# Optimization experiments

Measured on AMD Instinct MI355X. Metric: run time of the kernel, lower is better.

Reference implementation:

```python
import jax, jax.numpy as jnp
import numpy as np

D = 192          # d_model
H = 8            # n_heads
DH = D // H      # d_head = 24
DFF = 2 * D      # FeedForward hidden = d_model*2
SIZES = [384 + 8 * i for i in range(32)]   # ragged segment lengths
TOTAL = sum(SIZES)                          # 16256
EPS = 1e-5

# static ragged -> padded index maps (numpy, baked at trace time)
_sz = np.asarray(SIZES)
B = len(_sz)
MAXN = int(_sz.max())
SEG = np.repeat(np.arange(B), _sz)                      # [TOTAL] segment id
POS = np.concatenate([np.arange(s) for s in _sz])       # [TOTAL] position in segment
PADMASK = np.ones((B, MAXN), dtype=bool)                # True = padding (key_padding_mask)
PADMASK[SEG, POS] = False


def _layernorm(x, gamma, beta):
    mu = jnp.mean(x, axis=-1, keepdims=True)
    var = jnp.var(x, axis=-1, keepdims=True)
    return (x - mu) * jax.lax.rsqrt(var + EPS) * gamma + beta


def setup_inputs() -> dict:
    key = jax.random.key(0)
    ks = jax.random.split(key, 8)
    w = lambda k, shape: jax.random.normal(k, shape, jnp.float32) * 0.02
    return {
        "x": jax.random.normal(ks[0], (TOTAL, D), jnp.float32),
        "sizes": jnp.asarray(SIZES, jnp.int32),
        "Wqkv": w(ks[1], (3 * D, D)), "bqkv": jnp.zeros((3 * D,), jnp.float32),
        "Wo": w(ks[2], (D, D)),       "bo": jnp.zeros((D,), jnp.float32),
        "Wg": w(ks[3], (D, 2 * D)),   "bg": jnp.zeros((D,), jnp.float32),
        "gamma1": jnp.ones((D,), jnp.float32), "beta1": jnp.zeros((D,), jnp.float32),
        "W1": w(ks[4], (DFF, D)),     "b1": jnp.zeros((DFF,), jnp.float32),
        "W2": w(ks[5], (D, DFF)),     "b2": jnp.zeros((D,), jnp.float32),
        "gamma2": jnp.ones((D,), jnp.float32), "beta2": jnp.zeros((D,), jnp.float32),
    }


def reference(x, sizes, Wqkv, bqkv, Wo, bo, Wg, bg, gamma1, beta1,
              W1, b1, W2, b2, gamma2, beta2):
    # --- pad_by_sizes (vectorized scatter, static index maps) ---
    pad = jnp.zeros((B, MAXN, D), x.dtype).at[SEG, POS].set(x)   # [B, MAXN, D]

    # --- nn.MultiheadAttention (batch_first, key_padding_mask) ---
    qkv = pad @ Wqkv.T + bqkv                                    # [B, MAXN, 3D]
    q, k, v = jnp.split(qkv, 3, axis=-1)
    def heads(t):  # [B, MAXN, D] -> [B, H, MAXN, DH]
        return t.reshape(B, MAXN, H, DH).transpose(0, 2, 1, 3)
    q, k, v = heads(q), heads(k), heads(v)
    scores = jnp.einsum("bhqd,bhkd->bhqk", q, k) / np.sqrt(DH)   # [B, H, MAXN, MAXN]
    scores = jnp.where(PADMASK[:, None, None, :], jnp.float32(-1e9), scores)
    attn = jax.nn.softmax(scores, axis=-1)
    o = jnp.einsum("bhqk,bhkd->bhqd", attn, v)                   # [B, H, MAXN, DH]
    o = o.transpose(0, 2, 1, 3).reshape(B, MAXN, D)
    out = o @ Wo.T + bo                                          # [B, MAXN, D]

    # --- gather back to ragged; gate/norm/ff are per-token, so the torch
    # per-segment loop is equivalent to one vectorized pass over all tokens ---
    out_flat = out[SEG, POS]                                     # [TOTAL, D]
    g = jax.nn.sigmoid(jnp.concatenate([out_flat, x], axis=-1) @ Wg.T + bg)
    h = g * out_flat + (1.0 - g) * x                             # GatedResidual
    h = _layernorm(h, gamma1, beta1)                             # self.norm
    y = jax.nn.silu(h @ W1.T + b1) @ W2.T + b2                   # FeedForward.net
    return _layernorm(h + y, gamma2, beta2)                      # residual + norm
```

## Files before the change

### kernel.cpp

```cpp
#include <hip/hip_runtime.h>
#include <math.h>

#define D_      192
#define H_      8
#define DH_     24
#define NSEG    32
#define TOTAL_  16256
static constexpr float LN_EPS = 1e-5f;
static constexpr float SCALE  = 0.20412414523193154f;
static constexpr float SC_L2E = 0.29446679331797463f;

typedef float  f32x4  __attribute__((ext_vector_type(4)));
typedef short  bf16x8 __attribute__((ext_vector_type(8)));
typedef unsigned short u16x4 __attribute__((ext_vector_type(4)));
typedef unsigned int   u32x4 __attribute__((ext_vector_type(4)));

__device__ __forceinline__ unsigned short f2b(float f) {
    union { float f; unsigned u; } v; v.f = f;
    unsigned r = v.u + 0x7FFFu + ((v.u >> 16) & 1u);
    return (unsigned short)(r >> 16);
}
__device__ __forceinline__ unsigned f2b_u32(float f) {
    union { float f; unsigned u; } v; v.f = f;
    return (v.u + 0x8000u) >> 16;
}
__device__ __forceinline__ unsigned short f2b_fast(float f) {
    union { float f; unsigned u; } v; v.f = f;
    return (unsigned short)((v.u + 0x8000u) >> 16);
}
__device__ __forceinline__ float b2f(unsigned short h) {
    union { unsigned u; float f; } v; v.u = (unsigned)h << 16; return v.f;
}
__device__ __forceinline__ float fexp2(float x) {
#if __has_builtin(__builtin_amdgcn_exp2f)
    return __builtin_amdgcn_exp2f(x);
#else
    return exp2f(x);
#endif
}
__device__ __forceinline__ bf16x8 ldpack8(const float* p) {
    float4 a0 = *(const float4*)p;
    float4 a1 = *(const float4*)(p + 4);
    bf16x8 r;
    ((unsigned short*)&r)[0] = f2b(a0.x); ((unsigned short*)&r)[1] = f2b(a0.y);
    ((unsigned short*)&r)[2] = f2b(a0.z); ((unsigned short*)&r)[3] = f2b(a0.w);
    ((unsigned short*)&r)[4] = f2b(a1.x); ((unsigned short*)&r)[5] = f2b(a1.y);
    ((unsigned short*)&r)[6] = f2b(a1.z); ((unsigned short*)&r)[7] = f2b(a1.w);
    return r;
}

#define NXE 3121152
__global__ __launch_bounds__(256)
void conv_all(const float* __restrict__ x,
              const float* __restrict__ w0, const float* __restrict__ w1,
              const float* __restrict__ w2, const float* __restrict__ w3,
              const float* __restrict__ w4,
              unsigned short* __restrict__ xb, unsigned short* __restrict__ wb)
{
    int i = (blockIdx.x * 256 + threadIdx.x) * 4;
    const float* src; unsigned short* dst; int off;
    if (i < NXE) { src = x; dst = xb; off = 0; }
    else {
        int j = i - NXE; dst = wb;
        if      (j < 110592) { src = w0; off = 0; }
        else if (j < 147456) { src = w1; off = 110592; }
        else if (j < 221184) { src = w2; off = 147456; }
        else if (j < 294912) { src = w3; off = 221184; }
        else                 { src = w4; off = 294912; }
        i = j;
    }
    float4 v = *(const float4*)&src[i - off];
    u16x4 o = { f2b(v.x), f2b(v.y), f2b(v.z), f2b(v.w) };
    *(u16x4*)&dst[i] = o;
}

template<int KF, int MR, int OUT_BF16>
__global__ __launch_bounds__(256)
void gemm_lds(const unsigned short* __restrict__ Ain,
              const unsigned short* __restrict__ Wb,
              const float* __restrict__ bias,
              void* __restrict__ Cout, int N)
{
    constexpr int KSW = KF * 32 + 8;
    __shared__ unsigned short Wp[64 * KSW];

    const int tid = threadIdx.x;
    const int wv  = tid >> 6;
    const int l   = tid & 63;
    const int m0  = blockIdx.x * (64 * MR) + wv * (16 * MR);
    const int n0  = blockIdx.y * 64;
    const int rl  = l & 15;
    const int kc  = (l >> 4) * 8;

    bf16x8 afrag[MR][KF];
    #pragma unroll
    for (int h = 0; h < MR; ++h)
        #pragma unroll
        for (int kk = 0; kk < KF; ++kk)
            afrag[h][kk] = *(const bf16x8*)&Ain[(size_t)(m0 + h * 16 + rl) * (KF * 32) + kk * 32 + kc];

    #pragma unroll
    for (int i = 0; i < KF; ++i) {
        int u = i * 256 + tid;
        int row = u / (KF * 4), c = u % (KF * 4);
        *(bf16x8*)&Wp[row * KSW + c * 8] = *(const bf16x8*)&Wb[(size_t)(n0 + row) * (KF * 32) + c * 8];
    }
    __syncthreads();

    f32x4 acc[MR][4] = {};
    #pragma unroll
    for (int kk = 0; kk < KF; ++kk) {
        #pragma unroll
        for (int nf = 0; nf < 4; ++nf) {
            bf16x8 b = *(const bf16x8*)&Wp[(nf * 16 + rl) * KSW + kk * 32 + kc];
            #pragma unroll
            for (int h = 0; h < MR; ++h)
                acc[h][nf] = __builtin_amdgcn_mfma_f32_16x16x32_bf16(afrag[h][kk], b, acc[h][nf], 0, 0, 0);
        }
    }

    #pragma unroll
    for (int h = 0; h < MR; ++h) {
        #pragma unroll
        for (int nf = 0; nf < 4; ++nf) {
            const int c = n0 + nf * 16 + rl;
            const float bz = bias[c];
            #pragma unroll
            for (int q = 0; q < 4; ++q) {
                const int r = m0 + h * 16 + (l >> 4) * 4 + q;
                float v = acc[h][nf][q] + bz;
                if (OUT_BF16) ((unsigned short*)Cout)[(size_t)r * N + c] = f2b(v);
                else          ((float*)Cout)[(size_t)r * N + c] = v;
            }
        }
    }
}

__global__ __launch_bounds__(256, 1)
void wo_gate_ln1(const unsigned short* __restrict__ o_b,
                 const float* __restrict__ x,
                 const unsigned short* __restrict__ wo_b,
                 const unsigned short* __restrict__ wg_b,
                 const float* __restrict__ bo, const float* __restrict__ bg,
                 const float* __restrict__ gamma1, const float* __restrict__ beta1,
                 float* __restrict__ h1, unsigned short* __restrict__ h1b)
{
    constexpr int WS = 200;
    constexpr int AS = 200;
    __shared__ unsigned short Wp[192 * WS];
    __shared__ unsigned short Al[64 * AS];

    const int tid = threadIdx.x;
    const int wv  = tid >> 6;
    const int l   = tid & 63;
    const int rl  = l & 15;
    const int g   = l >> 4;
    const int kc  = g * 8;
    const int m0  = blockIdx.x * 64 + wv * 16;

    bf16x8 afA[6];
    #pragma unroll
    for (int kk = 0; kk < 6; ++kk)
        afA[kk] = *(const bf16x8*)&o_b[(size_t)(m0 + rl) * 192 + kk * 32 + kc];

    #pragma unroll
    for (int i = 0; i < 18; ++i) {
        int u = i * 256 + tid;
        int row = u / 24, c = u % 24;
        *(bf16x8*)&Wp[row * WS + c * 8] = *(const bf16x8*)&wo_b[(size_t)row * 192 + c * 8];
    }
    __syncthreads();

    f32x4 accA[12] = {};
    #pragma unroll
    for (int kk = 0; kk < 6; ++kk)
        #pragma unroll
        for (int nf = 0; nf < 12; ++nf) {
            bf16x8 b = *(const bf16x8*)&Wp[(nf * 16 + rl) * WS + kk * 32 + kc];
            accA[nf] = __builtin_amdgcn_mfma_f32_16x16x32_bf16(afA[kk], b, accA[nf], 0, 0, 0);
        }

    float att[12][4];
    #pragma unroll
    for (int nf = 0; nf < 12; ++nf) {
        const float bz = bo[nf * 16 + rl];
        #pragma unroll
        for (int q = 0; q < 4; ++q) {
            att[nf][q] = accA[nf][q] + bz;
            const int row = wv * 16 + g * 4 + q;
            Al[row * AS + nf * 16 + rl] = f2b(att[nf][q]);
        }
    }
    __syncthreads();

    #pragma unroll
    for (int i = 0; i < 18; ++i) {
        int u = i * 256 + tid;
        int row = u / 24, c = u % 24;
        *(bf16x8*)&Wp[row * WS + c * 8] = *(const bf16x8*)&wg_b[(size_t)row * 384 + c * 8];
    }
    __syncthreads();

    f32x4 accB[12] = {};
    #pragma unroll
    for (int kk = 0; kk < 6; ++kk) {
        bf16x8 a = *(const bf16x8*)&Al[(wv * 16 + rl) * AS + kk * 32 + kc];
        #pragma unroll
        for (int nf = 0; nf < 12; ++nf) {
            bf16x8 b = *(const bf16x8*)&Wp[(nf * 16 + rl) * WS + kk * 32 + kc];
            accB[nf] = __builtin_amdgcn_mfma_f32_16x16x32_bf16(a, b, accB[nf], 0, 0, 0);
        }
    }
    __syncthreads();

    #pragma unroll
    for (int i = 0; i < 18; ++i) {
        int u = i * 256 + tid;
        int row = u / 24, c = u % 24;
        *(bf16x8*)&Wp[row * WS + c * 8] = *(const bf16x8*)&wg_b[(size_t)row * 384 + 192 + c * 8];
    }
    __syncthreads();

    #pragma unroll
    for (int kk = 0; kk < 6; ++kk) {
        bf16x8 a = ldpack8(&x[(size_t)(m0 + rl) * 192 + kk * 32 + kc]);
        #pragma unroll
        for (int nf = 0; nf < 12; ++nf) {
            bf16x8 b = *(const bf16x8*)&Wp[(nf * 16 + rl) * WS + kk * 32 + kc];
            accB[nf] = __builtin_amdgcn_mfma_f32_16x16x32_bf16(a, b, accB[nf], 0, 0, 0);
        }
    }

    float bz[12], gam[12], bet[12];
    #pragma unroll
    for (int nf = 0; nf < 12; ++nf) {
        bz[nf]  = bg[nf * 16 + rl];
        gam[nf] = gamma1[nf * 16 + rl];
        bet[nf] = beta1[nf * 16 + rl];
    }
    #pragma unroll
    for (int q = 0; q < 4; ++q) {
        const int r = m0 + g * 4 + q;
        const size_t rb = (size_t)r * 192;
        float h[12];
        float s = 0.f;
        #pragma unroll
        for (int nf = 0; nf < 12; ++nf) {
            const int c = nf * 16 + rl;
            float v  = accB[nf][q] + bz[nf];
            float gt = 1.f / (1.f + __expf(-v));
            h[nf] = gt * att[nf][q] + (1.f - gt) * x[rb + c];
            s += h[nf];
        }
        s += __shfl_xor(s, 1); s += __shfl_xor(s, 2);
        s += __shfl_xor(s, 4); s += __shfl_xor(s, 8);
        const float mu = s * (1.f / 192.f);
        float sq = 0.f;
        #pragma unroll
        for (int nf = 0; nf < 12; ++nf) { float d = h[nf] - mu; sq += d * d; }
        sq += __shfl_xor(sq, 1); sq += __shfl_xor(sq, 2);
        sq += __shfl_xor(sq, 4); sq += __shfl_xor(sq, 8);
        const float rstd = rsqrtf(sq * (1.f / 192.f) + LN_EPS);
        #pragma unroll
        for (int nf = 0; nf < 12; ++nf) {
            const int c = nf * 16 + rl;
            float rv = (h[nf] - mu) * rstd * gam[nf] + bet[nf];
            h1[rb + c]  = rv;
            h1b[rb + c] = f2b(rv);
        }
    }
}

__global__ __launch_bounds__(256, 1)
void ffn_ln2(const unsigned short* __restrict__ h1b,
             const float* __restrict__ h1,
             const unsigned short* __restrict__ w1_b,
             const unsigned short* __restrict__ w2_b,
             const float* __restrict__ b1, const float* __restrict__ b2,
             const float* __restrict__ gamma2, const float* __restrict__ beta2,
             float* __restrict__ out)
{
    constexpr int WS = 200;
    constexpr int FS = 392;
    __shared__ unsigned short Wp[192 * WS];
    __shared__ unsigned short Fl[64 * FS];

    const int tid = threadIdx.x;
    const int wv  = tid >> 6;
    const int l   = tid & 63;
    const int rl  = l & 15;
    const int g   = l >> 4;
    const int kc  = g * 8;
    const int m0  = blockIdx.x * 64 + wv * 16;

    bf16x8 afC[6];
    #pragma unroll
    for (int kk = 0; kk < 6; ++kk)
        afC[kk] = *(const bf16x8*)&h1b[(size_t)(m0 + rl) * 192 + kk * 32 + kc];

    f32x4 accC[24] = {};
    #pragma unroll
    for (int ch = 0; ch < 2; ++ch) {
        if (ch) __syncthreads();
        #pragma unroll
        for (int i = 0; i < 18; ++i) {
            int u = i * 256 + tid;
            int row = u / 24, c = u % 24;
            *(bf16x8*)&Wp[row * WS + c * 8] = *(const bf16x8*)&w1_b[(size_t)(ch * 192 + row) * 192 + c * 8];
        }
        __syncthreads();
        #pragma unroll
        for (int kk = 0; kk < 6; ++kk)
            #pragma unroll
            for (int nf = 0; nf < 12; ++nf) {
                bf16x8 b = *(const bf16x8*)&Wp[(nf * 16 + rl) * WS + kk * 32 + kc];
                accC[ch * 12 + nf] = __builtin_amdgcn_mfma_f32_16x16x32_bf16(afC[kk], b, accC[ch * 12 + nf], 0, 0, 0);
            }
    }
    #pragma unroll
    for (int ch = 0; ch < 2; ++ch)
        #pragma unroll
        for (int nf = 0; nf < 12; ++nf) {
            const int col = ch * 192 + nf * 16 + rl;
            const float bz = b1[col];
            #pragma unroll
            for (int q = 0; q < 4; ++q) {
                float v = accC[ch * 12 + nf][q] + bz;
                float s = 1.f / (1.f + __expf(-v));
                const int row = wv * 16 + g * 4 + q;
                Fl[row * FS + col] = f2b(v * s);
            }
        }
    __syncthreads();

    f32x4 accD[12] = {};
    #pragma unroll
    for (int ch = 0; ch < 2; ++ch) {
        if (ch) __syncthreads();
        #pragma unroll
        for (int i = 0; i < 18; ++i) {
            int u = i * 256 + tid;
            int row = u / 24, c = u % 24;
            *(bf16x8*)&Wp[row * WS + c * 8] = *(const bf16x8*)&w2_b[(size_t)row * 384 + ch * 192 + c * 8];
        }
        __syncthreads();
        #pragma unroll
        for (int kk = 0; kk < 6; ++kk) {
            bf16x8 a = *(const bf16x8*)&Fl[(wv * 16 + rl) * FS + ch * 192 + kk * 32 + kc];
            #pragma unroll
            for (int nf = 0; nf < 12; ++nf) {
                bf16x8 b = *(const bf16x8*)&Wp[(nf * 16 + rl) * WS + kk * 32 + kc];
                accD[nf] = __builtin_amdgcn_mfma_f32_16x16x32_bf16(a, b, accD[nf], 0, 0, 0);
            }
        }
    }

    float bz[12], gam[12], bet[12];
    #pragma unroll
    for (int nf = 0; nf < 12; ++nf) {
        bz[nf]  = b2[nf * 16 + rl];
        gam[nf] = gamma2[nf * 16 + rl];
        bet[nf] = beta2[nf * 16 + rl];
    }
    #pragma unroll
    for (int q = 0; q < 4; ++q) {
        const int r = m0 + g * 4 + q;
        const size_t rb = (size_t)r * 192;
        float h[12];
        float s = 0.f;
        #pragma unroll
        for (int nf = 0; nf < 12; ++nf) {
            const int c = nf * 16 + rl;
            h[nf] = h1[rb + c] + accD[nf][q] + bz[nf];
            s += h[nf];
        }
        s += __shfl_xor(s, 1); s += __shfl_xor(s, 2);
        s += __shfl_xor(s, 4); s += __shfl_xor(s, 8);
        const float mu = s * (1.f / 192.f);
        float sq = 0.f;
        #pragma unroll
        for (int nf = 0; nf < 12; ++nf) { float d = h[nf] - mu; sq += d * d; }
        sq += __shfl_xor(sq, 1); sq += __shfl_xor(sq, 2);
        sq += __shfl_xor(sq, 4); sq += __shfl_xor(sq, 8);
        const float rstd = rsqrtf(sq * (1.f / 192.f) + LN_EPS);
        #pragma unroll
        for (int nf = 0; nf < 12; ++nf) {
            const int c = nf * 16 + rl;
            out[rb + c] = (h[nf] - mu) * rstd * gam[nf] + bet[nf];
        }
    }
}

#define KSTR 40
#define VSTR 72

__global__ __launch_bounds__(256)
void attn_mfma(const unsigned short* __restrict__ qkv, unsigned short* __restrict__ o)
{
    const int seg  = blockIdx.z;
    const int head = blockIdx.y;
    const int n    = 384 + 8 * seg;
    const int base = 384 * seg + 4 * seg * (seg - 1);
    const int q0   = blockIdx.x * 128;
    if (q0 >= n) return;

    __shared__ unsigned short Ks[64 * KSTR];
    __shared__ unsigned short Vt[32 * VSTR];

    const int tid = threadIdx.x;
    const int wv  = tid >> 6;
    const int l   = tid & 63;
    const int lq  = l & 15;
    const int g   = l >> 4;

    if (tid < 64) *(uint4*)&Ks[tid * KSTR + 24] = make_uint4(0, 0, 0, 0);
    for (int t4 = tid; t4 < 144; t4 += 256)
        *(unsigned long long*)&Vt[24 * VSTR + t4 * 4] = 0ull;

    int   qrow[2];
    bf16x8 qfrag[2];
    #pragma unroll
    for (int qf = 0; qf < 2; ++qf) {
        qrow[qf] = q0 + wv * 32 + qf * 16 + lq;
        const int qtok = base + (qrow[qf] < n ? qrow[qf] : n - 1);
        bf16x8 qz = {};
        if (g < 3) qz = *(const bf16x8*)&qkv[(size_t)qtok * 576 + head * 24 + g * 8];
        qfrag[qf] = qz;
    }

    float lsum[2] = {0.f, 0.f};
    f32x4 oacc[2][2] = {};

    const int nt = (n + 63) >> 6;
    for (int t = 0; t < nt; ++t) {
        const int j0 = t * 64;
        __syncthreads();
        if (tid < 192) {
            const int j = tid & 63;
            const int c = tid >> 6;
            const int cj = 32 * (j >> 5) + 8 * ((j >> 2) & 3) + 4 * ((j >> 4) & 1) + (j & 3);
            int jr = j0 + j; if (jr >= n) jr = n - 1;
            const unsigned short* rp = &qkv[(size_t)(base + jr) * 576 + head * 24 + c * 8];
            bf16x8 kv = *(const bf16x8*)(rp + 192);
            *(bf16x8*)&Ks[j * KSTR + c * 8] = kv;
            bf16x8 vv = *(const bf16x8*)(rp + 384);
            #pragma unroll
            for (int e = 0; e < 8; ++e)
                Vt[(c * 8 + e) * VSTR + cj] = ((const unsigned short*)&vv)[e];
        }
        __syncthreads();

        bf16x8 kf[4];
        #pragma unroll
        for (int ks = 0; ks < 4; ++ks)
            kf[ks] = *(const bf16x8*)&Ks[(ks * 16 + lq) * KSTR + g * 8];

        const int rem = n - j0;
        bf16x8 pfr[2][2];
        #pragma unroll
        for (int qf = 0; qf < 2; ++qf) {
            f32x4 sacc[4] = {};
            #pragma unroll
            for (int ks = 0; ks < 4; ++ks)
                sacc[ks] = __builtin_amdgcn_mfma_f32_16x16x32_bf16(kf[ks], qfrag[qf], sacc[ks], 0, 0, 0);

            float psum = 0.f;
            unsigned pw[8];
            #pragma unroll
            for (int ks = 0; ks < 4; ++ks) {
                float pv[4];
                #pragma unroll
                for (int r = 0; r < 4; ++r) {
                    float p = fexp2(sacc[ks][r] * SC_L2E);
                    if (rem < 64) { int key = ks * 16 + g * 4 + r; if (key >= rem) p = 0.f; }
                    psum += p;
                    pv[r] = p;
                }
                pw[ks * 2 + 0] = f2b_u32(pv[0]) | (f2b_u32(pv[1]) << 16);
                pw[ks * 2 + 1] = f2b_u32(pv[2]) | (f2b_u32(pv[3]) << 16);
            }
            psum += __shfl_xor(psum, 16);
            psum += __shfl_xor(psum, 32);
            lsum[qf] += psum;
            #pragma unroll
            for (int jk = 0; jk < 2; ++jk) {
                u32x4 fr = { pw[jk*4+0], pw[jk*4+1], pw[jk*4+2], pw[jk*4+3] };
                pfr[qf][jk] = *(bf16x8*)&fr;
            }
        }

        #pragma unroll
        for (int jk = 0; jk < 2; ++jk) {
            bf16x8 vf[2];
            #pragma unroll
            for (int df = 0; df < 2; ++df)
                vf[df] = *(const bf16x8*)&Vt[(df * 16 + lq) * VSTR + jk * 32 + g * 8];
            #pragma unroll
            for (int qf = 0; qf < 2; ++qf)
                #pragma unroll
                for (int df = 0; df < 2; ++df)
                    oacc[qf][df] = __builtin_amdgcn_mfma_f32_16x16x32_bf16(vf[df], pfr[qf][jk], oacc[qf][df], 0, 0, 0);
        }
    }

    #pragma unroll
    for (int qf = 0; qf < 2; ++qf) {
        if (qrow[qf] < n) {
            const float rl2 = 1.f / lsum[qf];
            #pragma unroll
            for (int df = 0; df < 2; ++df) {
                const int d0 = df * 16 + g * 4;
                if (d0 < 24) {
                    u16x4 r = { f2b_fast(oacc[qf][df][0] * rl2), f2b_fast(oacc[qf][df][1] * rl2),
                                f2b_fast(oacc[qf][df][2] * rl2), f2b_fast(oacc[qf][df][3] * rl2) };
                    *(u16x4*)&o[(size_t)(base + qrow[qf]) * 192 + head * 24 + d0] = r;
                }
            }
        }
    }
}

extern "C" void kernel_launch(void* const* d_in, const int* in_sizes, int n_in,
                              void* d_out, int out_size, void* d_ws, size_t ws_size,
                              hipStream_t stream)
{
    const float* x      = (const float*)d_in[0];
    const float* Wqkv   = (const float*)d_in[2];
    const float* bqkv   = (const float*)d_in[3];
    const float* Wo     = (const float*)d_in[4];
    const float* bo     = (const float*)d_in[5];
    const float* Wg     = (const float*)d_in[6];
    const float* bg     = (const float*)d_in[7];
    const float* gamma1 = (const float*)d_in[8];
    const float* beta1  = (const float*)d_in[9];
    const float* W1     = (const float*)d_in[10];
    const float* b1     = (const float*)d_in[11];
    const float* W2     = (const float*)d_in[12];
    const float* b2     = (const float*)d_in[13];
    const float* gamma2 = (const float*)d_in[14];
    const float* beta2  = (const float*)d_in[15];
    float* out = (float*)d_out;
    float* ws  = (float*)d_ws;

    const size_t T = TOTAL_;
    unsigned short* qkv_b = (unsigned short*)ws;
    unsigned short* o_b   = (unsigned short*)(ws + 288 * T);
    float*          h1    = ws + 384 * T;
    unsigned short* h1b   = (unsigned short*)(ws + 576 * T);
    unsigned short* wb    = (unsigned short*)(ws + 672 * T);
    unsigned short* xb    = (unsigned short*)(ws + 684 * T);

    dim3 blk(256);

    conv_all<<<dim3(3408), blk, 0, stream>>>(x, Wqkv, Wo, Wg, W1, W2, xb, wb);
    gemm_lds<6,2,1><<<dim3(127, 9), blk, 0, stream>>>(xb, wb, bqkv, qkv_b, 576);
    attn_mfma<<<dim3(5, H_, NSEG), blk, 0, stream>>>(qkv_b, o_b);
    wo_gate_ln1<<<dim3(254), blk, 0, stream>>>(o_b, x, wb + 110592, wb + 147456,
                                               bo, bg, gamma1, beta1, h1, h1b);
    ffn_ln2<<<dim3(254), blk, 0, stream>>>(h1b, h1, wb + 221184, wb + 294912,
                                           b1, b2, gamma2, beta2, out);
}
```

Measured before the change: 97.69 us.

## Double-buffer attention K/V tiles, halve LDS in MLP kernels, drop fp32 intermediates

```diff
diff --git a/kernel.cpp b/kernel.cpp
--- a/kernel.cpp
+++ b/kernel.cpp
@@ -37,16 +37,6 @@
 #else
     return exp2f(x);
 #endif
-}
-__device__ __forceinline__ bf16x8 ldpack8(const float* p) {
-    float4 a0 = *(const float4*)p;
-    float4 a1 = *(const float4*)(p + 4);
-    bf16x8 r;
-    ((unsigned short*)&r)[0] = f2b(a0.x); ((unsigned short*)&r)[1] = f2b(a0.y);
-    ((unsigned short*)&r)[2] = f2b(a0.z); ((unsigned short*)&r)[3] = f2b(a0.w);
-    ((unsigned short*)&r)[4] = f2b(a1.x); ((unsigned short*)&r)[5] = f2b(a1.y);
-    ((unsigned short*)&r)[6] = f2b(a1.z); ((unsigned short*)&r)[7] = f2b(a1.w);
-    return r;
 }
 
 #define NXE 3121152
@@ -136,19 +126,18 @@
     }
 }
 
-__global__ __launch_bounds__(256, 1)
+__global__ __launch_bounds__(256, 2)
 void wo_gate_ln1(const unsigned short* __restrict__ o_b,
-                 const float* __restrict__ x,
+                 const unsigned short* __restrict__ xb,
                  const unsigned short* __restrict__ wo_b,
                  const unsigned short* __restrict__ wg_b,
                  const float* __restrict__ bo, const float* __restrict__ bg,
                  const float* __restrict__ gamma1, const float* __restrict__ beta1,
-                 float* __restrict__ h1, unsigned short* __restrict__ h1b)
+                 unsigned short* __restrict__ h1b)
 {
     constexpr int WS = 200;
-    constexpr int AS = 200;
-    __shared__ unsigned short Wp[192 * WS];
-    __shared__ unsigned short Al[64 * AS];
+    __shared__ unsigned short Wp[96 * WS];
+    __shared__ unsigned short Al[64 * WS];
 
     const int tid = threadIdx.x;
     const int wv  = tid >> 6;
@@ -163,80 +152,75 @@
     for (int kk = 0; kk < 6; ++kk)
         afA[kk] = *(const bf16x8*)&o_b[(size_t)(m0 + rl) * 192 + kk * 32 + kc];
 
-    #pragma unroll
-    for (int i = 0; i < 18; ++i) {
-        int u = i * 256 + tid;
-        int row = u / 24, c = u % 24;
-        *(bf16x8*)&Wp[row * WS + c * 8] = *(const bf16x8*)&wo_b[(size_t)row * 192 + c * 8];
-    }
-    __syncthreads();
-
     f32x4 accA[12] = {};
     #pragma unroll
-    for (int kk = 0; kk < 6; ++kk)
-        #pragma unroll
-        for (int nf = 0; nf < 12; ++nf) {
-            bf16x8 b = *(const bf16x8*)&Wp[(nf * 16 + rl) * WS + kk * 32 + kc];
-            accA[nf] = __builtin_amdgcn_mfma_f32_16x16x32_bf16(afA[kk], b, accA[nf], 0, 0, 0);
-        }
+    for (int sub = 0; sub < 2; ++sub) {
+        __syncthreads();
+        #pragma unroll
+        for (int i = 0; i < 9; ++i) {
+            int u = i * 256 + tid;
+            int row = u / 24, c = u % 24;
+            *(bf16x8*)&Wp[row * WS + c * 8] = *(const bf16x8*)&wo_b[(size_t)(sub * 96 + row) * 192 + c * 8];
+        }
+        __syncthreads();
+        #pragma unroll
+        for (int kk = 0; kk < 6; ++kk)
+            #pragma unroll
+            for (int nf2 = 0; nf2 < 6; ++nf2) {
+                bf16x8 b = *(const bf16x8*)&Wp[(nf2 * 16 + rl) * WS + kk * 32 + kc];
+                accA[sub * 6 + nf2] = __builtin_amdgcn_mfma_f32_16x16x32_bf16(afA[kk], b, accA[sub * 6 + nf2], 0, 0, 0);
+            }
+    }
 
     float att[12][4];
     #pragma unroll
     for (int nf = 0; nf < 12; ++nf) {
-        const float bz = bo[nf * 16 + rl];
+        const int cnf = (nf / 6) * 96 + (nf % 6) * 16 + rl;
+        const float bz = bo[cnf];
         #pragma unroll
         for (int q = 0; q < 4; ++q) {
             att[nf][q] = accA[nf][q] + bz;
-            const int row = wv * 16 + g * 4 + q;
-            Al[row * AS + nf * 16 + rl] = f2b(att[nf][q]);
-        }
-    }
-    __syncthreads();
-
-    #pragma unroll
-    for (int i = 0; i < 18; ++i) {
-        int u = i * 256 + tid;
-        int row = u / 24, c = u % 24;
-        *(bf16x8*)&Wp[row * WS + c * 8] = *(const bf16x8*)&wg_b[(size_t)row * 384 + c * 8];
-    }
-    __syncthreads();
+            Al[(wv * 16 + g * 4 + q) * WS + cnf] = f2b(att[nf][q]);
+        }
+    }
+
+    bf16x8 afX[6];
+    #pragma unroll
+    for (int kk = 0; kk < 6; ++kk)
+        afX[kk] = *(const bf16x8*)&xb[(size_t)(m0 + rl) * 192 + kk * 32 + kc];
 
     f32x4 accB[12] = {};
     #pragma unroll
-    for (int kk = 0; kk < 6; ++kk) {
-        bf16x8 a = *(const bf16x8*)&Al[(wv * 16 + rl) * AS + kk * 32 + kc];
-        #pragma unroll
-        for (int nf = 0; nf < 12; ++nf) {
-            bf16x8 b = *(const bf16x8*)&Wp[(nf * 16 + rl) * WS + kk * 32 + kc];
-            accB[nf] = __builtin_amdgcn_mfma_f32_16x16x32_bf16(a, b, accB[nf], 0, 0, 0);
-        }
-    }
-    __syncthreads();
-
-    #pragma unroll
-    for (int i = 0; i < 18; ++i) {
-        int u = i * 256 + tid;
-        int row = u / 24, c = u % 24;
-        *(bf16x8*)&Wp[row * WS + c * 8] = *(const bf16x8*)&wg_b[(size_t)row * 384 + 192 + c * 8];
-    }
-    __syncthreads();
-
-    #pragma unroll
-    for (int kk = 0; kk < 6; ++kk) {
-        bf16x8 a = ldpack8(&x[(size_t)(m0 + rl) * 192 + kk * 32 + kc]);
-        #pragma unroll
-        for (int nf = 0; nf < 12; ++nf) {
-            bf16x8 b = *(const bf16x8*)&Wp[(nf * 16 + rl) * WS + kk * 32 + kc];
-            accB[nf] = __builtin_amdgcn_mfma_f32_16x16x32_bf16(a, b, accB[nf], 0, 0, 0);
-        }
-    }
+    for (int kb = 0; kb < 2; ++kb)
+        #pragma unroll
+        for (int sub = 0; sub < 2; ++sub) {
+            __syncthreads();
+            #pragma unroll
+            for (int i = 0; i < 9; ++i) {
+                int u = i * 256 + tid;
+                int row = u / 24, c = u % 24;
+                *(bf16x8*)&Wp[row * WS + c * 8] = *(const bf16x8*)&wg_b[(size_t)(sub * 96 + row) * 384 + kb * 192 + c * 8];
+            }
+            __syncthreads();
+            #pragma unroll
+            for (int kk = 0; kk < 6; ++kk) {
+                bf16x8 a = (kb == 0) ? *(const bf16x8*)&Al[(wv * 16 + rl) * WS + kk * 32 + kc]
+                                     : afX[kk];
+                #pragma unroll
+                for (int nf2 = 0; nf2 < 6; ++nf2) {
+                    bf16x8 b = *(const bf16x8*)&Wp[(nf2 * 16 + rl) * WS + kk * 32 + kc];
+                    accB[sub * 6 + nf2] = __builtin_amdgcn_mfma_f32_16x16x32_bf16(a, b, accB[sub * 6 + nf2], 0, 0, 0);
+                }
+            }
+        }
 
     float bz[12], gam[12], bet[12];
     #pragma unroll
     for (int nf = 0; nf < 12; ++nf) {
-        bz[nf]  = bg[nf * 16 + rl];
-        gam[nf] = gamma1[nf * 16 + rl];
-        bet[nf] = beta1[nf * 16 + rl];
+        const int cnf = (nf / 6) * 96 + (nf % 6) * 16 + rl;
+        bz[nf]  = bg[cnf];
+        gam[nf] = gamma1[cnf];
+        bet[nf] = beta1[cnf];
     }
     #pragma unroll
     for (int q = 0; q < 4; ++q) {
@@ -246,10 +230,10 @@
         float s = 0.f;
         #pragma unroll
         for (int nf = 0; nf < 12; ++nf) {
-            const int c = nf * 16 + rl;
+            const int cnf = (nf / 6) * 96 + (nf % 6) * 16 + rl;
             float v  = accB[nf][q] + bz[nf];
             float gt = 1.f / (1.f + __expf(-v));
-            h[nf] = gt * att[nf][q] + (1.f - gt) * x[rb + c];
+            h[nf] = gt * att[nf][q] + (1.f - gt) * b2f(xb[rb + cnf]);
             s += h[nf];
         }
         s += __shfl_xor(s, 1); s += __shfl_xor(s, 2);
@@ -263,17 +247,14 @@
         const float rstd = rsqrtf(sq * (1.f / 192.f) + LN_EPS);
         #pragma unroll
         for (int nf = 0; nf < 12; ++nf) {
-            const int c = nf * 16 + rl;
-            float rv = (h[nf] - mu) * rstd * gam[nf] + bet[nf];
-            h1[rb + c]  = rv;
-            h1b[rb + c] = f2b(rv);
-        }
-    }
-}
-
-__global__ __launch_bounds__(256, 1)
+            const int cnf = (nf / 6) * 96 + (nf % 6) * 16 + rl;
+            h1b[rb + cnf] = f2b((h[nf] - mu) * rstd * gam[nf] + bet[nf]);
+        }
+    }
+}
+
+__global__ __launch_bounds__(256, 2)
 void ffn_ln2(const unsigned short* __restrict__ h1b,
-             const float* __restrict__ h1,
              const unsigned short* __restrict__ w1_b,
              const unsigned short* __restrict__ w2_b,
              const float* __restrict__ b1, const float* __restrict__ b2,
@@ -281,9 +262,8 @@
              float* __restrict__ out)
 {
     constexpr int WS = 200;
-    constexpr int FS = 392;
-    __shared__ unsigned short Wp[192 * WS];
-    __shared__ unsigned short Fl[64 * FS];
+    __shared__ unsigned short Wp[96 * WS];
+    __shared__ unsigned short Fl[64 * WS];
 
     const int tid = threadIdx.x;
     const int wv  = tid >> 6;
@@ -298,59 +278,57 @@
     for (int kk = 0; kk < 6; ++kk)
         afC[kk] = *(const bf16x8*)&h1b[(size_t)(m0 + rl) * 192 + kk * 32 + kc];
 
-    f32x4 accC[24] = {};
+    f32x4 accD[12] = {};
     #pragma unroll
     for (int ch = 0; ch < 2; ++ch) {
-        if (ch) __syncthreads();
-        #pragma unroll
-        for (int i = 0; i < 18; ++i) {
-            int u = i * 256 + tid;
-            int row = u / 24, c = u % 24;
-            *(bf16x8*)&Wp[row * WS + c * 8] = *(const bf16x8*)&w1_b[(size_t)(ch * 192 + row) * 192 + c * 8];
-        }
-        __syncthreads();
-        #pragma unroll
-        for (int kk = 0; kk < 6; ++kk)
-            #pragma unroll
-            for (int nf = 0; nf < 12; ++nf) {
-                bf16x8 b = *(const bf16x8*)&Wp[(nf * 16 + rl) * WS + kk * 32 + kc];
-                accC[ch * 12 + nf] = __builtin_amdgcn_mfma_f32_16x16x32_bf16(afC[kk], b, accC[ch * 12 + nf], 0, 0, 0);
-            }
-    }
-    #pragma unroll
-    for (int ch = 0; ch < 2; ++ch)
+        f32x4 accC[12] = {};
+        #pragma unroll
+        for (int sub = 0; sub < 2; ++sub) {
+            __syncthreads();
+            #pragma unroll
+            for (int i = 0; i < 9; ++i) {
+                int u = i * 256 + tid;
+                int row = u / 24, c = u % 24;
+                *(bf16x8*)&Wp[row * WS + c * 8] = *(const bf16x8*)&w1_b[(size_t)(ch * 192 + sub * 96 + row) * 192 + c * 8];
+            }
+            __syncthreads();
+            #pragma unroll
+            for (int kk = 0; kk < 6; ++kk)
+                #pragma unroll
+                for (int nf2 = 0; nf2 < 6; ++nf2) {
+                    bf16x8 b = *(const bf16x8*)&Wp[(nf2 * 16 + rl) * WS + kk * 32 + kc];
+                    accC[sub * 6 + nf2] = __builtin_amdgcn_mfma_f32_16x16x32_bf16(afC[kk], b, accC[sub * 6 + nf2], 0, 0, 0);
+                }
+        }
         #pragma unroll
         for (int nf = 0; nf < 12; ++nf) {
-            const int col = ch * 192 + nf * 16 + rl;
-            const float bz = b1[col];
+            const int colc = (nf / 6) * 96 + (nf % 6) * 16 + rl;
+            const float bz1 = b1[ch * 192 + colc];
             #pragma unroll
             for (int q = 0; q < 4; ++q) {
-                float v = accC[ch * 12 + nf][q] + bz;
+                float v = accC[nf][q] + bz1;
                 float s = 1.f / (1.f + __expf(-v));
-                const int row = wv * 16 + g * 4 + q;
-                Fl[row * FS + col] = f2b(v * s);
-            }
-        }
-    __syncthreads();
-
-    f32x4 accD[12] = {};
-    #pragma unroll
-    for (int ch = 0; ch < 2; ++ch) {
-        if (ch) __syncthreads();
-        #pragma unroll
-        for (int i = 0; i < 18; ++i) {
-            int u = i * 256 + tid;
-            int row = u / 24, c = u % 24;
-            *(bf16x8*)&Wp[row * WS + c * 8] = *(const bf16x8*)&w2_b[(size_t)row * 384 + ch * 192 + c * 8];
-        }
-        __syncthreads();
-        #pragma unroll
-        for (int kk = 0; kk < 6; ++kk) {
-            bf16x8 a = *(const bf16x8*)&Fl[(wv * 16 + rl) * FS + ch * 192 + kk * 32 + kc];
-            #pragma unroll
-            for (int nf = 0; nf < 12; ++nf) {
-                bf16x8 b = *(const bf16x8*)&Wp[(nf * 16 + rl) * WS + kk * 32 + kc];
-                accD[nf] = __builtin_amdgcn_mfma_f32_16x16x32_bf16(a, b, accD[nf], 0, 0, 0);
+                Fl[(wv * 16 + g * 4 + q) * WS + colc] = f2b(v * s);
+            }
+        }
+        #pragma unroll
+        for (int sub = 0; sub < 2; ++sub) {
+            __syncthreads();
+            #pragma unroll
+            for (int i = 0; i < 9; ++i) {
+                int u = i * 256 + tid;
+                int row = u / 24, c = u % 24;
+                *(bf16x8*)&Wp[row * WS + c * 8] = *(const bf16x8*)&w2_b[(size_t)(sub * 96 + row) * 384 + ch * 192 + c * 8];
+            }
+            __syncthreads();
+            #pragma unroll
+            for (int kk = 0; kk < 6; ++kk) {
+                bf16x8 a = *(const bf16x8*)&Fl[(wv * 16 + rl) * WS + kk * 32 + kc];
+                #pragma unroll
+                for (int nf2 = 0; nf2 < 6; ++nf2) {
+                    bf16x8 b = *(const bf16x8*)&Wp[(nf2 * 16 + rl) * WS + kk * 32 + kc];
+                    accD[sub * 6 + nf2] = __builtin_amdgcn_mfma_f32_16x16x32_bf16(a, b, accD[sub * 6 + nf2], 0, 0, 0);
+                }
             }
         }
     }
@@ -358,9 +336,10 @@
     float bz[12], gam[12], bet[12];
     #pragma unroll
     for (int nf = 0; nf < 12; ++nf) {
-        bz[nf]  = b2[nf * 16 + rl];
-        gam[nf] = gamma2[nf * 16 + rl];
-        bet[nf] = beta2[nf * 16 + rl];
+        const int cnf = (nf / 6) * 96 + (nf % 6) * 16 + rl;
+        bz[nf]  = b2[cnf];
+        gam[nf] = gamma2[cnf];
+        bet[nf] = beta2[cnf];
     }
     #pragma unroll
     for (int q = 0; q < 4; ++q) {
@@ -370,8 +349,8 @@
         float s = 0.f;
         #pragma unroll
         for (int nf = 0; nf < 12; ++nf) {
-            const int c = nf * 16 + rl;
-            h[nf] = h1[rb + c] + accD[nf][q] + bz[nf];
+            const int cnf = (nf / 6) * 96 + (nf % 6) * 16 + rl;
+            h[nf] = b2f(h1b[rb + cnf]) + accD[nf][q] + bz[nf];
             s += h[nf];
         }
         s += __shfl_xor(s, 1); s += __shfl_xor(s, 2);
@@ -385,8 +364,8 @@
         const float rstd = rsqrtf(sq * (1.f / 192.f) + LN_EPS);
         #pragma unroll
         for (int nf = 0; nf < 12; ++nf) {
-            const int c = nf * 16 + rl;
-            out[rb + c] = (h[nf] - mu) * rstd * gam[nf] + bet[nf];
+            const int cnf = (nf / 6) * 96 + (nf % 6) * 16 + rl;
+            out[rb + cnf] = (h[nf] - mu) * rstd * gam[nf] + bet[nf];
         }
     }
 }
@@ -404,8 +383,8 @@
     const int q0   = blockIdx.x * 128;
     if (q0 >= n) return;
 
-    __shared__ unsigned short Ks[64 * KSTR];
-    __shared__ unsigned short Vt[32 * VSTR];
+    __shared__ unsigned short Ks[2][64 * KSTR];
+    __shared__ unsigned short Vt[2][32 * VSTR];
 
     const int tid = threadIdx.x;
     const int wv  = tid >> 6;
@@ -413,9 +392,14 @@
     const int lq  = l & 15;
     const int g   = l >> 4;
 
-    if (tid < 64) *(uint4*)&Ks[tid * KSTR + 24] = make_uint4(0, 0, 0, 0);
-    for (int t4 = tid; t4 < 144; t4 += 256)
-        *(unsigned long long*)&Vt[24 * VSTR + t4 * 4] = 0ull;
+    if (tid < 64) {
+        *(uint4*)&Ks[0][tid * KSTR + 24] = make_uint4(0, 0, 0, 0);
+        *(uint4*)&Ks[1][tid * KSTR + 24] = make_uint4(0, 0, 0, 0);
+    }
+    for (int t4 = tid; t4 < 144; t4 += 256) {
+        *(unsigned long long*)&Vt[0][24 * VSTR + t4 * 4] = 0ull;
+        *(unsigned long long*)&Vt[1][24 * VSTR + t4 * 4] = 0ull;
+    }
 
     int   qrow[2];
     bf16x8 qfrag[2];
@@ -428,32 +412,42 @@
         qfrag[qf] = qz;
     }
 
+    const int sj  = tid & 63;
+    const int sc  = tid >> 6;
+    const int scj = 32 * (sj >> 5) + 8 * ((sj >> 2) & 3) + 4 * ((sj >> 4) & 1) + (sj & 3);
+
+    bf16x8 kreg = {}, vreg = {};
+    if (tid < 192) {
+        int jr = sj; if (jr >= n) jr = n - 1;
+        const unsigned short* rp = &qkv[(size_t)(base + jr) * 576 + head * 24 + sc * 8];
+        kreg = *(const bf16x8*)(rp + 192);
+        vreg = *(const bf16x8*)(rp + 384);
+        *(bf16x8*)&Ks[0][sj * KSTR + sc * 8] = kreg;
+        #pragma unroll
+        for (int e = 0; e < 8; ++e)
+            Vt[0][(sc * 8 + e) * VSTR + scj] = ((const unsigned short*)&vreg)[e];
+    }
+
     float lsum[2] = {0.f, 0.f};
     f32x4 oacc[2][2] = {};
 
     const int nt = (n + 63) >> 6;
+    int cur = 0;
     for (int t = 0; t < nt; ++t) {
+        __syncthreads();
         const int j0 = t * 64;
-        __syncthreads();
-        if (tid < 192) {
-            const int j = tid & 63;
-            const int c = tid >> 6;
-            const int cj = 32 * (j >> 5) + 8 * ((j >> 2) & 3) + 4 * ((j >> 4) & 1) + (j & 3);
-            int jr = j0 + j; if (jr >= n) jr = n - 1;
-            const unsigned short* rp = &qkv[(size_t)(base + jr) * 576 + head * 24 + c * 8];
-            bf16x8 kv = *(const bf16x8*)(rp + 192);
-            *(bf16x8*)&Ks[j * KSTR + c * 8] = kv;
-            bf16x8 vv = *(const bf16x8*)(rp + 384);
-            #pragma unroll
-            for (int e = 0; e < 8; ++e)
-                Vt[(c * 8 + e) * VSTR + cj] = ((const unsigned short*)&vv)[e];
-        }
-        __syncthreads();
+        const bool pf = (t + 1 < nt) && (tid < 192);
+        if (pf) {
+            int jr = j0 + 64 + sj; if (jr >= n) jr = n - 1;
+            const unsigned short* rp = &qkv[(size_t)(base + jr) * 576 + head * 24 + sc * 8];
+            kreg = *(const bf16x8*)(rp + 192);
+            vreg = *(const bf16x8*)(rp + 384);
+        }
 
         bf16x8 kf[4];
         #pragma unroll
         for (int ks = 0; ks < 4; ++ks)
-            kf[ks] = *(const bf16x8*)&Ks[(ks * 16 + lq) * KSTR + g * 8];
+            kf[ks] = *(const bf16x8*)&Ks[cur][(ks * 16 + lq) * KSTR + g * 8];
 
         const int rem = n - j0;
         bf16x8 pfr[2][2];
@@ -494,13 +488,21 @@
             bf16x8 vf[2];
             #pragma unroll
             for (int df = 0; df < 2; ++df)
-                vf[df] = *(const bf16x8*)&Vt[(df * 16 + lq) * VSTR + jk * 32 + g * 8];
+                vf[df] = *(const bf16x8*)&Vt[cur][(df * 16 + lq) * VSTR + jk * 32 + g * 8];
             #pragma unroll
             for (int qf = 0; qf < 2; ++qf)
                 #pragma unroll
                 for (int df = 0; df < 2; ++df)
                     oacc[qf][df] = __builtin_amdgcn_mfma_f32_16x16x32_bf16(vf[df], pfr[qf][jk], oacc[qf][df], 0, 0, 0);
         }
+
+        if (pf) {
+            *(bf16x8*)&Ks[cur ^ 1][sj * KSTR + sc * 8] = kreg;
+            #pragma unroll
+            for (int e = 0; e < 8; ++e)
+                Vt[cur ^ 1][(sc * 8 + e) * VSTR + scj] = ((const unsigned short*)&vreg)[e];
+        }
+        cur ^= 1;
     }
 
     #pragma unroll
@@ -545,18 +547,17 @@
     const size_t T = TOTAL_;
     unsigned short* qkv_b = (unsigned short*)ws;
     unsigned short* o_b   = (unsigned short*)(ws + 288 * T);
-    float*          h1    = ws + 384 * T;
-    unsigned short* h1b   = (unsigned short*)(ws + 576 * T);
-    unsigned short* wb    = (unsigned short*)(ws + 672 * T);
-    unsigned short* xb    = (unsigned short*)(ws + 684 * T);
+    unsigned short* h1b   = (unsigned short*)(ws + 384 * T);
+    unsigned short* wb    = (unsigned short*)(ws + 480 * T);
+    unsigned short* xb    = (unsigned short*)(ws + 492 * T);
 
     dim3 blk(256);
 
     conv_all<<<dim3(3408), blk, 0, stream>>>(x, Wqkv, Wo, Wg, W1, W2, xb, wb);
     gemm_lds<6,2,1><<<dim3(127, 9), blk, 0, stream>>>(xb, wb, bqkv, qkv_b, 576);
     attn_mfma<<<dim3(5, H_, NSEG), blk, 0, stream>>>(qkv_b, o_b);
-    wo_gate_ln1<<<dim3(254), blk, 0, stream>>>(o_b, x, wb + 110592, wb + 147456,
-                                               bo, bg, gamma1, beta1, h1, h1b);
-    ffn_ln2<<<dim3(254), blk, 0, stream>>>(h1b, h1, wb + 221184, wb + 294912,
+    wo_gate_ln1<<<dim3(254), blk, 0, stream>>>(o_b, xb, wb + 110592, wb + 147456,
+                                               bo, bg, gamma1, beta1, h1b);
+    ffn_ln2<<<dim3(254), blk, 0, stream>>>(h1b, wb + 221184, wb + 294912,
                                            b1, b2, gamma2, beta2, out);
 }
```

Measured after the change: 99.19 us. Within noise of the previous version (+1.5%).
